# Kernel tuning notes

Hardware: AMD Instinct MI355X
Metric: run time of the kernel (lower is better)

## Reference

```python
import jax, jax.numpy as jnp
import numpy as np

B, H, D = 8, 1024, 4
K_COUP = 1.0
DT = 1.0


def setup_inputs() -> dict:
    key = jax.random.key(0)
    k1, k2, k3, k4, k5 = jax.random.split(key, 5)
    return {
        "theta_prev": jax.random.normal(k1, (B, H, D), dtype=jnp.float32),
        "gamma": jax.random.normal(k2, (B, H), dtype=jnp.float32),
        "A": jax.random.normal(k3, (B, H, H), dtype=jnp.float32),
        "omega": jax.random.normal(k4, (H, D), dtype=jnp.float32) * 0.1,
        "kappa": jnp.ones((H, D), dtype=jnp.float32),
        "alpha": jax.random.normal(k5, (H, H), dtype=jnp.float32) * 0.1,
    }


def reference(theta_prev, gamma, A, omega, kappa, alpha):
    # theta_prev: [B,H,D], gamma: [B,H], A: [B,H,H]
    Bn, Hn, Dn = theta_prev.shape
    # symmetrize + relu lateral coupling matrix
    A_lat = jax.nn.relu(0.5 * (A + jnp.swapaxes(A, 1, 2)))  # [B,H,H]
    # pairwise phase differences: theta_j - theta_i - alpha -> [B,H,H,D]
    phase_diff = (theta_prev[:, None, :, :] - theta_prev[:, :, None, :]
                  - alpha[None, :, :, None])
    # weighted sum over j axis
    coupling = (K_COUP / Hn) * jnp.sum(A_lat[..., None] * jnp.sin(phase_diff), axis=2)  # [B,H,D]
    theta_dot = omega[None] + coupling + kappa[None] * (gamma[..., None] - theta_prev)
    return theta_prev + DT * theta_dot
```

## Files before the change

### kernel.cpp

```cpp
#include <hip/hip_runtime.h>
#include <math.h>

#define BB 8
#define HH 1024
#define DD 4
#define TI 16
#define NJC 8
#define JC (HH / NJC)


__global__ __launch_bounds__(256, 8) void kuramoto_partial(
    const float* __restrict__ theta, const float* __restrict__ A,
    const float* __restrict__ alpha, float* __restrict__ ws)
{
    const int blk = blockIdx.x;
    const int jc  = blk & (NJC - 1);
    const int it  = (blk >> 3) & 63;
    const int b   = blk >> 9;
    const int i0  = it * TI;
    const int j0  = jc * JC;
    const int t   = threadIdx.x;
    const int ti  = t >> 4;
    const int tj  = t & 15;

    __shared__ float sTh0[JC], sTh1[JC], sTh2[JC], sTh3[JC];
    __shared__ float sAT[JC][TI + 1];

    const float* Ab = A + (size_t)b * HH * HH;

    if (t < JC) {
        const float4 v = ((const float4*)theta)[(size_t)b * HH + j0 + t];
        sTh0[t] = v.x; sTh1[t] = v.y; sTh2[t] = v.z; sTh3[t] = v.w;
    }

    {
        const int r = t >> 2;
        const int c = (t & 3) * 4;
        #pragma unroll
        for (int rr = 0; rr < JC; rr += 64) {
            const int row = rr + r;
            const float4 v = *(const float4*)&Ab[(size_t)(j0 + row) * HH + i0 + c];
            sAT[row][c + 0] = v.x;
            sAT[row][c + 1] = v.y;
            sAT[row][c + 2] = v.z;
            sAT[row][c + 3] = v.w;
        }
    }
    __syncthreads();

    const float4 thi = ((const float4*)theta)[(size_t)b * HH + i0 + ti];
    const float4* Arow4  = (const float4*)(Ab    + (size_t)(i0 + ti) * HH + j0);
    const float4* alrow4 = (const float4*)(alpha + (size_t)(i0 + ti) * HH + j0);

    float a0 = 0.f, a1 = 0.f, a2 = 0.f, a3 = 0.f;

    #pragma unroll
    for (int s = 0; s < JC / 64; ++s) {
        const int q = tj + 16 * s;
        const float4 ad = Arow4[q];
        const float4 al = alrow4[q];
        const int j = 4 * q;
        #pragma unroll
        for (int k = 0; k < 4; ++k) {
            const float adk = (&ad.x)[k];
            const float alk = (&al.x)[k];
            const float at  = sAT[j + k][ti];
            const float alat = fmaxf(0.5f * (adk + at), 0.0f);
            a0 += alat * __sinf(sTh0[j + k] - thi.x - alk);
            a1 += alat * __sinf(sTh1[j + k] - thi.y - alk);
            a2 += alat * __sinf(sTh2[j + k] - thi.z - alk);
            a3 += alat * __sinf(sTh3[j + k] - thi.w - alk);
        }
    }

    #pragma unroll
    for (int off = 8; off >= 1; off >>= 1) {
        a0 += __shfl_down(a0, off, 16);
        a1 += __shfl_down(a1, off, 16);
        a2 += __shfl_down(a2, off, 16);
        a3 += __shfl_down(a3, off, 16);
    }

    if (tj == 0) {
        float4 r; r.x = a0; r.y = a1; r.z = a2; r.w = a3;
        ((float4*)ws)[((size_t)jc * BB + b) * HH + i0 + ti] = r;
    }
}

__global__ __launch_bounds__(256) void kuramoto_final(
    const float* __restrict__ theta, const float* __restrict__ gamma,
    const float* __restrict__ omega, const float* __restrict__ kappa,
    const float* __restrict__ ws, float* __restrict__ out)
{
    const int idx = blockIdx.x * 256 + threadIdx.x;
    const int i   = idx & (HH - 1);
    const float4* w4 = (const float4*)ws;

    float4 p = w4[idx];
    #pragma unroll
    for (int jc = 1; jc < NJC; ++jc) {
        const float4 q = w4[(size_t)jc * BB * HH + idx];
        p.x += q.x; p.y += q.y; p.z += q.z; p.w += q.w;
    }

    const float4 th = ((const float4*)theta)[idx];
    const float4 om = ((const float4*)omega)[i];
    const float4 kp = ((const float4*)kappa)[i];
    const float  g  = gamma[idx];
    const float  inv = 1.0f / HH;

    float4 o;
    o.x = th.x + om.x + p.x * inv + kp.x * (g - th.x);
    o.y = th.y + om.y + p.y * inv + kp.y * (g - th.y);
    o.z = th.z + om.z + p.z * inv + kp.z * (g - th.z);
    o.w = th.w + om.w + p.w * inv + kp.w * (g - th.w);
    ((float4*)out)[idx] = o;
}

extern "C" void kernel_launch(void* const* d_in, const int* in_sizes, int n_in,
                              void* d_out, int out_size, void* d_ws, size_t ws_size,
                              hipStream_t stream) {
    const float* theta = (const float*)d_in[0];
    const float* gamma = (const float*)d_in[1];
    const float* A     = (const float*)d_in[2];
    const float* omega = (const float*)d_in[3];
    const float* kappa = (const float*)d_in[4];
    const float* alpha = (const float*)d_in[5];
    float* out = (float*)d_out;
    float* ws  = (float*)d_ws;

    hipLaunchKernelGGL(kuramoto_partial, dim3(BB * (HH / TI) * NJC), dim3(256), 0, stream,
                       theta, A, alpha, ws);
    hipLaunchKernelGGL(kuramoto_final, dim3(BB * HH / 256), dim3(256), 0, stream,
                       theta, gamma, omega, kappa, ws, out);
}
```

Before: 93.18 us.

## Process two query rows per thread and use native scaled hardware sine

Each thread now handles two i rows (tile of 32 instead of 16), so every shared-memory theta_j load is reused twice and the grid is halved. Angles are prescaled by 1/(2π) so the raw hardware sine instruction (v_sin_f32, which takes revolutions) can be called without the range multiply. The 0.5 symmetrization factor is folded into the final scaling constant. The cost is more registers per thread and possibly lower occupancy, plus slight precision differences from the prescaled angles.

After: 109.7 us. +17.8%, slower.

```diff
diff --git a/kernel.cpp b/kernel.cpp
--- a/kernel.cpp
+++ b/kernel.cpp
@@ -4,9 +4,10 @@
 #define BB 8
 #define HH 1024
 #define DD 4
-#define TI 16
+#define TI2 32
 #define NJC 8
 #define JC (HH / NJC)
+#define INV2PI 0.15915494309189535f
 
 
 __global__ __launch_bounds__(256, 8) void kuramoto_partial(
@@ -15,29 +16,30 @@
 {
     const int blk = blockIdx.x;
     const int jc  = blk & (NJC - 1);
-    const int it  = (blk >> 3) & 63;
-    const int b   = blk >> 9;
-    const int i0  = it * TI;
+    const int it  = (blk >> 3) & 31;
+    const int b   = blk >> 8;
+    const int i0  = it * TI2;
     const int j0  = jc * JC;
     const int t   = threadIdx.x;
     const int ti  = t >> 4;
     const int tj  = t & 15;
 
+    __shared__ float sAT[JC][TI2 + 1];
     __shared__ float sTh0[JC], sTh1[JC], sTh2[JC], sTh3[JC];
-    __shared__ float sAT[JC][TI + 1];
 
     const float* Ab = A + (size_t)b * HH * HH;
 
     if (t < JC) {
         const float4 v = ((const float4*)theta)[(size_t)b * HH + j0 + t];
-        sTh0[t] = v.x; sTh1[t] = v.y; sTh2[t] = v.z; sTh3[t] = v.w;
+        sTh0[t] = v.x * INV2PI; sTh1[t] = v.y * INV2PI;
+        sTh2[t] = v.z * INV2PI; sTh3[t] = v.w * INV2PI;
     }
 
     {
-        const int r = t >> 2;
-        const int c = (t & 3) * 4;
+        const int r = t >> 3;
+        const int c = (t & 7) * 4;
         #pragma unroll
-        for (int rr = 0; rr < JC; rr += 64) {
+        for (int rr = 0; rr < JC; rr += 32) {
             const int row = rr + r;
             const float4 v = *(const float4*)&Ab[(size_t)(j0 + row) * HH + i0 + c];
             sAT[row][c + 0] = v.x;
@@ -46,30 +48,52 @@
             sAT[row][c + 3] = v.w;
         }
     }
+
+    float4 thia = ((const float4*)theta)[(size_t)b * HH + i0 + ti];
+    float4 thib = ((const float4*)theta)[(size_t)b * HH + i0 + ti + 16];
+    thia.x *= INV2PI; thia.y *= INV2PI; thia.z *= INV2PI; thia.w *= INV2PI;
+    thib.x *= INV2PI; thib.y *= INV2PI; thib.z *= INV2PI; thib.w *= INV2PI;
+
     __syncthreads();
 
-    const float4 thi = ((const float4*)theta)[(size_t)b * HH + i0 + ti];
-    const float4* Arow4  = (const float4*)(Ab    + (size_t)(i0 + ti) * HH + j0);
-    const float4* alrow4 = (const float4*)(alpha + (size_t)(i0 + ti) * HH + j0);
+    const float4* Ara = (const float4*)(Ab    + (size_t)(i0 + ti)      * HH + j0);
+    const float4* Arb = (const float4*)(Ab    + (size_t)(i0 + ti + 16) * HH + j0);
+    const float4* ala = (const float4*)(alpha + (size_t)(i0 + ti)      * HH + j0);
+    const float4* alb = (const float4*)(alpha + (size_t)(i0 + ti + 16) * HH + j0);
 
     float a0 = 0.f, a1 = 0.f, a2 = 0.f, a3 = 0.f;
+    float b0 = 0.f, b1 = 0.f, b2 = 0.f, b3 = 0.f;
 
     #pragma unroll
     for (int s = 0; s < JC / 64; ++s) {
         const int q = tj + 16 * s;
-        const float4 ad = Arow4[q];
-        const float4 al = alrow4[q];
-        const int j = 4 * q;
+        const float4 ad_a = Ara[q];
+        const float4 ad_b = Arb[q];
+        const float4 al_a = ala[q];
+        const float4 al_b = alb[q];
         #pragma unroll
         for (int k = 0; k < 4; ++k) {
-            const float adk = (&ad.x)[k];
-            const float alk = (&al.x)[k];
-            const float at  = sAT[j + k][ti];
-            const float alat = fmaxf(0.5f * (adk + at), 0.0f);
-            a0 += alat * __sinf(sTh0[j + k] - thi.x - alk);
-            a1 += alat * __sinf(sTh1[j + k] - thi.y - alk);
-            a2 += alat * __sinf(sTh2[j + k] - thi.z - alk);
-            a3 += alat * __sinf(sTh3[j + k] - thi.w - alk);
+            const int j = 4 * q + k;
+            const float t0 = sTh0[j];
+            const float t1 = sTh1[j];
+            const float t2 = sTh2[j];
+            const float t3 = sTh3[j];
+            {
+                const float alat = fmaxf((&ad_a.x)[k] + sAT[j][ti], 0.0f);
+                const float w    = (&al_a.x)[k] * INV2PI;
+                a0 += alat * __builtin_amdgcn_sinf(t0 - thia.x - w);
+                a1 += alat * __builtin_amdgcn_sinf(t1 - thia.y - w);
+                a2 += alat * __builtin_amdgcn_sinf(t2 - thia.z - w);
+                a3 += alat * __builtin_amdgcn_sinf(t3 - thia.w - w);
+            }
+            {
+                const float alat = fmaxf((&ad_b.x)[k] + sAT[j][ti + 16], 0.0f);
+                const float w    = (&al_b.x)[k] * INV2PI;
+                b0 += alat * __builtin_amdgcn_sinf(t0 - thib.x - w);
+                b1 += alat * __builtin_amdgcn_sinf(t1 - thib.y - w);
+                b2 += alat * __builtin_amdgcn_sinf(t2 - thib.z - w);
+                b3 += alat * __builtin_amdgcn_sinf(t3 - thib.w - w);
+            }
         }
     }
 
@@ -79,11 +103,18 @@
         a1 += __shfl_down(a1, off, 16);
         a2 += __shfl_down(a2, off, 16);
         a3 += __shfl_down(a3, off, 16);
+        b0 += __shfl_down(b0, off, 16);
+        b1 += __shfl_down(b1, off, 16);
+        b2 += __shfl_down(b2, off, 16);
+        b3 += __shfl_down(b3, off, 16);
     }
 
     if (tj == 0) {
-        float4 r; r.x = a0; r.y = a1; r.z = a2; r.w = a3;
-        ((float4*)ws)[((size_t)jc * BB + b) * HH + i0 + ti] = r;
+        float4 ra; ra.x = a0; ra.y = a1; ra.z = a2; ra.w = a3;
+        float4 rb; rb.x = b0; rb.y = b1; rb.z = b2; rb.w = b3;
+        float4* w4 = (float4*)ws + ((size_t)jc * BB + b) * HH;
+        w4[i0 + ti]      = ra;
+        w4[i0 + ti + 16] = rb;
     }
 }
 
@@ -107,7 +138,7 @@
     const float4 om = ((const float4*)omega)[i];
     const float4 kp = ((const float4*)kappa)[i];
     const float  g  = gamma[idx];
-    const float  inv = 1.0f / HH;
+    const float  inv = 0.5f / HH;
 
     float4 o;
     o.x = th.x + om.x + p.x * inv + kp.x * (g - th.x);
@@ -129,7 +160,7 @@
     float* out = (float*)d_out;
     float* ws  = (float*)d_ws;
 
-    hipLaunchKernelGGL(kuramoto_partial, dim3(BB * (HH / TI) * NJC), dim3(256), 0, stream,
+    hipLaunchKernelGGL(kuramoto_partial, dim3(BB * (HH / TI2) * NJC), dim3(256), 0, stream,
                        theta, A, alpha, ws);
     hipLaunchKernelGGL(kuramoto_final, dim3(BB * HH / 256), dim3(256), 0, stream,
                        theta, gamma, omega, kappa, ws, out);
```
